# Kernel optimization log

Hardware: AMD Instinct MI355X
Metric: run time of the kernel (lower is better)

The kernel has to match this reference:

```python
import jax, jax.numpy as jnp
import numpy as np

N_NODES = 65536
N_FEAT = 64
N_EDGES = 1048576
N_GRAPHS = 16
LP_ITERS = 30


def setup_inputs() -> dict:
    key = jax.random.key(0)
    k1, k2, k3 = jax.random.split(key, 3)
    x = jax.random.normal(k1, (N_NODES, N_FEAT), dtype=jnp.float32)
    edge_index = jax.random.randint(k2, (2, N_EDGES), 0, N_NODES, dtype=jnp.int32)
    batch = jnp.sort(jax.random.randint(k3, (N_NODES,), 0, N_GRAPHS, dtype=jnp.int32))
    v2 = jnp.full((1,), 3.5, dtype=jnp.float32)  # learnable affinity scale param
    return {"x": x, "edge_index": edge_index, "batch": batch, "v2": v2}


def _lp_clustering(row, col, aff, n_nodes, n_iters):
    """Label propagation: each node adopts the neighbor label with max summed affinity."""
    E = row.shape[0]
    aff = jax.lax.stop_gradient(aff)  # clustering is discrete, no grad path

    def body(_, labels):
        lab_c = labels[col]                                    # neighbor labels per edge
        order = jnp.lexsort((lab_c, row))                      # sort by (row, neighbor-label)
        r_s, l_s, w_s = row[order], lab_c[order], aff[order]
        new_grp = jnp.concatenate([jnp.ones((1,), bool),
                                   (r_s[1:] != r_s[:-1]) | (l_s[1:] != l_s[:-1])])
        gid = jnp.cumsum(new_grp) - 1                          # dense (row,label) group ids
        gsum = jax.ops.segment_sum(w_s, gid, num_segments=E)   # affinity mass per group
        gcnt = jax.ops.segment_sum(jnp.ones_like(w_s), gid, num_segments=E)
        valid = gcnt > 0
        g_row = jnp.where(valid, jax.ops.segment_max(r_s, gid, num_segments=E), 0)
        g_lab = jnp.where(valid, jax.ops.segment_max(l_s, gid, num_segments=E), n_nodes)
        node_max = jax.ops.segment_max(jnp.where(valid, gsum, -jnp.inf), g_row,
                                       num_segments=n_nodes)
        win = valid & (gsum == node_max[g_row])
        # smallest winning label == torch argmax first-hit tie-break
        return jax.ops.segment_min(jnp.where(win, g_lab, n_nodes), g_row,
                                   num_segments=n_nodes)

    labels0 = jnp.arange(n_nodes, dtype=row.dtype)
    return jax.lax.fori_loop(0, n_iters, body, labels0)


def _forward(x, edge_index, batch, v2):
    n = x.shape[0]
    loops = jnp.arange(n, dtype=edge_index.dtype)
    ei = jnp.concatenate([edge_index, jnp.stack([loops, loops])], axis=1)  # add_self_loops
    row, col = ei[0], ei[1]

    # P2-style affinities: log_aff = -v2 * ||x_i - x_j||^2 ; forward exponentiates
    sqdist = jnp.sum((x[row] - x[col]) ** 2, axis=1)  # [E]
    losses = jnp.mean(sqdist)
    aff = jnp.exp(-v2[0] * sqdist)

    node_labels = _lp_clustering(row, col, aff, n, LP_ITERS)

    # unique(return_inverse): dense relabel of surviving cluster ids (sorted order)
    present = jnp.zeros((n,), jnp.int32).at[node_labels].set(1)
    cluster_labels = (jnp.cumsum(present) - 1)[node_labels]

    # max_pool_x: scatter-max node features into clusters (padded to n rows)
    cx = jax.ops.segment_max(x, cluster_labels, num_segments=n)
    cb = jax.ops.segment_max(batch, cluster_labels, num_segments=n)
    nonempty = jax.ops.segment_sum(jnp.ones((n,), jnp.int32), cluster_labels,
                                   num_segments=n) > 0
    cx = jnp.where(nonempty[:, None], cx, 0.0)
    cb = jnp.where(nonempty, cb, -1)

    # coalesce(cluster_labels[edge_index]): sort + dedupe, duplicates padded with -1
    mr, mc = cluster_labels[row], cluster_labels[col]
    order = jnp.lexsort((mc, mr))
    mr_s, mc_s = mr[order], mc[order]
    dup = jnp.concatenate([jnp.zeros((1,), bool),
                           (mr_s[1:] == mr_s[:-1]) & (mc_s[1:] == mc_s[:-1])])
    cei = jnp.stack([jnp.where(dup, -1, mr_s), jnp.where(dup, -1, mc_s)])

    return cx, cei, cb, cluster_labels, losses


def reference(x, edge_index, batch, v2):
    return _forward(x, edge_index, batch, v2)
```

## Files before the change

### kernel.cpp

```cpp
#include <hip/hip_runtime.h>
#include <hip/hip_cooperative_groups.h>

namespace cg = cooperative_groups;

#define DI __device__ __forceinline__

constexpr int NN   = 65536;
constexpr int NF   = 64;
constexpr int E0c  = 1048576;
constexpr int ET   = E0c + NN;
constexpr int LPITERS = 30;
constexpr int KPOS = 16;
constexpr int MSCH = 4096;
constexpr int NCHK = ET / MSCH;
constexpr int SCAP = 8192;
constexpr int CAP0 = 6144;
constexpr int BPB  = CAP0 / 64;
constexpr int NPART2 = 256 * BPB;

constexpr int O_CX   = 0;
constexpr int O_CEI0 = NN * NF;
constexpr int O_CEI1 = O_CEI0 + ET;
constexpr int O_CB   = O_CEI0 + 2 * ET;
constexpr int O_CL   = O_CB + NN;
constexpr int O_LOSS = O_CL + NN;

constexpr int W_CHG   = 0;
constexpr int W_NCLUS = 32;
constexpr int W_H1    = 64;
constexpr int W_GC0   = W_H1 + 256;
constexpr int W_GC1   = W_GC0 + 256;
constexpr int W_SCP   = 832;
constexpr int W_SCO   = W_SCP + 256;
constexpr int W_PART  = W_SCO + 256;
constexpr int W_PCNT  = W_PART + NPART2;
constexpr int W_PCOL  = W_PCNT + NN;
constexpr int W_PW    = W_PCOL + NN*KPOS;
constexpr int W_L0    = W_PW + NN*KPOS;
constexpr int W_L1    = W_L0 + NN;
constexpr int W_PRES  = W_L1 + NN;
constexpr int W_PSUM  = W_PRES + NN;
constexpr int W_CLU   = W_PSUM + NN;
constexpr int W_CBA   = W_CLU + NN;
constexpr int W_K0    = W_CBA + NN;
constexpr int W_K1    = W_K0 + 256*CAP0;

DI void edge_rc(const int* ei, int e, int& r, int& c) {
  if (e < E0c) { r = ei[e]; c = ei[E0c + e]; }
  else         { r = e - E0c; c = r; }
}

DI unsigned fenc(float f) {
  unsigned u = __float_as_uint(f);
  return (u & 0x80000000u) ? ~u : (u | 0x80000000u);
}
DI float fdec(unsigned u) {
  u = (u & 0x80000000u) ? (u & 0x7fffffffu) : ~u;
  return __uint_as_float(u);
}

DI int lp_step(int r, int d, int c0, int c1, float q0, float q1,
               const int* __restrict__ pcol, const float* __restrict__ pw,
               const int* __restrict__ lin) {
  int bl = NN;
  if (d == 1) {
    bl = lin[c0];
  } else if (d == 2) {
    int l0 = lin[c0], l1 = lin[c1];
    if (l0 == l1) bl = l0;
    else if (q1 > q0 || (q1 == q0 && l1 < l0)) bl = l1;
    else bl = l0;
  } else if (d > 2) {
    float best = 0.f;
    for (int i = 0; i < d; ++i) {
      int li = lin[pcol[r * KPOS + i]];
      bool dup = false;
      for (int j = 0; j < i; ++j)
        if (lin[pcol[r * KPOS + j]] == li) { dup = true; break; }
      if (dup) continue;
      float sum = 0.f;
      for (int j = i; j < d; ++j)
        if (lin[pcol[r * KPOS + j]] == li) sum += pw[r * KPOS + j];
      if (sum > best || (sum == best && li < bl)) { best = sum; bl = li; }
    }
  }
  return bl;
}


__global__ __launch_bounds__(256) void init_small(int* ws) {
  for (int i = threadIdx.x; i < 832; i += 256) ws[i] = 0;
}

__global__ __launch_bounds__(256) void emultisplit(const int* __restrict__ ei,
                                                   int* __restrict__ gcur0,
                                                   unsigned* __restrict__ K0,
                                                   int* __restrict__ pcnt,
                                                   int* __restrict__ L0) {
  __shared__ unsigned skey[MSCH];
  __shared__ unsigned short binid[MSCH];
  __shared__ int hl[256], ss[256], hs[256], hc[256], gb[256];
  int t = threadIdx.x;
  if (blockIdx.x < 256) {
    int rr = blockIdx.x * 256 + t;
    pcnt[rr] = 0;
    L0[rr] = rr;
  }
  hl[t] = 0; __syncthreads();
  int base = blockIdx.x * MSCH;
  unsigned mykey[MSCH / 256];
  #pragma unroll
  for (int k = 0; k < MSCH / 256; ++k) {
    int e = base + k * 256 + t;
    int r, c; edge_rc(ei, e, r, c);
    unsigned key = ((unsigned)r << 16) | (unsigned)c;
    mykey[k] = key;
    atomicAdd(&hl[key >> 24], 1);
  }
  __syncthreads();
  int v = hl[t];
  ss[t] = v; __syncthreads();
  for (int off = 1; off < 256; off <<= 1) {
    int u = (t >= off) ? ss[t - off] : 0;
    __syncthreads();
    ss[t] += u;
    __syncthreads();
  }
  int excl = ss[t] - v;
  hs[t] = excl;
  hc[t] = excl;
  gb[t] = t * CAP0 + ((v > 0) ? atomicAdd(&gcur0[t], v) : 0);
  for (int j = excl; j < excl + v; ++j) binid[j] = (unsigned short)t;
  __syncthreads();
  #pragma unroll
  for (int k = 0; k < MSCH / 256; ++k) {
    int b = mykey[k] >> 24;
    int slot = atomicAdd(&hc[b], 1);
    skey[slot] = mykey[k];
  }
  __syncthreads();
  for (int i = t; i < MSCH; i += 256) {
    int b = binid[i];
    int pos = gb[b] + (i - hs[b]);
    if (pos < (b + 1) * CAP0) K0[pos] = skey[i];
  }
}

__global__ __launch_bounds__(256) void edge_pos2(const float* __restrict__ x,
                                                 const unsigned* __restrict__ K0,
                                                 const int* __restrict__ gcur0,
                                                 const float* __restrict__ v2,
                                                 float* __restrict__ part,
                                                 int* __restrict__ pcnt,
                                                 int* __restrict__ pcol,
                                                 float* __restrict__ pw) {
  __shared__ float ls[16];
  int t = threadIdx.x, sub = t >> 4, lane = t & 15;
  int bkt = blockIdx.x / BPB;
  int off = (blockIdx.x % BPB) * 64;
  int cnt = gcur0[bkt];
  float w = v2[0];
  unsigned kk[4]; bool act[4];
  float4 A[4], B[4];
  #pragma unroll
  for (int q = 0; q < 4; ++q) {
    int j = off + sub * 4 + q;
    act[q] = (j < cnt);
    kk[q] = K0[bkt * CAP0 + (act[q] ? j : 0)];
  }
  #pragma unroll
  for (int q = 0; q < 4; ++q) {
    int r = kk[q] >> 16, c = kk[q] & 0xFFFF;
    A[q] = ((const float4*)(x + (size_t)r * NF))[lane];
    B[q] = ((const float4*)(x + (size_t)c * NF))[lane];
  }
  __builtin_amdgcn_sched_barrier(0);
  float lsum = 0.f;
  #pragma unroll
  for (int q = 0; q < 4; ++q) {
    float dx = A[q].x - B[q].x, dy = A[q].y - B[q].y;
    float dz = A[q].z - B[q].z, dw = A[q].w - B[q].w;
    float s = dx * dx + dy * dy + dz * dz + dw * dw;
    #pragma unroll
    for (int m = 1; m < 16; m <<= 1) s += __shfl_xor(s, m, 16);
    if (lane == 0 && act[q]) {
      lsum += s;
      float aff = expf(-w * s);
      if (aff > 0.f) {
        int r = kk[q] >> 16, c = kk[q] & 0xFFFF;
        int slot = atomicAdd(&pcnt[r], 1);
        if (slot < KPOS) { pcol[r * KPOS + slot] = c; pw[r * KPOS + slot] = aff; }
      }
    }
  }
  if (lane == 0) ls[sub] = lsum;
  __syncthreads();
  if (t == 0) {
    float s = 0.f;
    #pragma unroll
    for (int k = 0; k < 16; ++k) s += ls[k];
    part[blockIdx.x] = s;
  }
}

__global__ __launch_bounds__(256) void lp_iter0(const int* __restrict__ pcnt,
                                                const int* __restrict__ pcol,
                                                const float* __restrict__ pw,
                                                const int* __restrict__ L0,
                                                int* __restrict__ L1,
                                                int* __restrict__ chg,
                                                const float* __restrict__ part,
                                                float* __restrict__ out_loss) {
  __shared__ float smf[256];
  int t = threadIdx.x;
  int r = blockIdx.x * 256 + t;
  int d = pcnt[r];
  if (d > KPOS) d = KPOS;
  int c0 = 0, c1 = 0; float q0 = 0.f, q1 = 0.f;
  if (d >= 1) { c0 = pcol[r * KPOS];     q0 = pw[r * KPOS]; }
  if (d >= 2) { c1 = pcol[r * KPOS + 1]; q1 = pw[r * KPOS + 1]; }
  int bl = lp_step(r, d, c0, c1, q0, q1, pcol, pw, L0);
  L1[r] = bl;
  if (bl != L0[r]) atomicOr(&chg[0], 1);
  if (blockIdx.x == 0) {
    float s = 0.f;
    for (int i = t; i < NPART2; i += 256) s += part[i];
    smf[t] = s; __syncthreads();
    for (int off = 128; off; off >>= 1) {
      if (t < off) smf[t] += smf[t + off];
      __syncthreads();
    }
    if (t == 0) out_loss[0] = smf[0] / (float)ET;
  }
}

__global__ __launch_bounds__(256) void general_tail(
    const int* __restrict__ pcnt, const int* __restrict__ pcol,
    const float* __restrict__ pw, int* __restrict__ L0, int* __restrict__ L1,
    int* __restrict__ chg, int* __restrict__ pres, int* __restrict__ psum,
    int* __restrict__ clu, float* __restrict__ out_cl, int* __restrict__ cba,
    unsigned* __restrict__ cxacc, const float* __restrict__ x,
    const int* __restrict__ batch, int* __restrict__ nclus_g,
    int* __restrict__ scp, int* __restrict__ sco, int* __restrict__ h1,
    const int* __restrict__ gcur0, int* __restrict__ gcur1,
    const unsigned* __restrict__ K0, unsigned* __restrict__ K1,
    float* __restrict__ out_cb) {
  if (chg[0] == 0) return;
  __shared__ int sm[256], hl[256], bases[256];
  __shared__ int sbc;
  cg::grid_group grid = cg::this_grid();
  int t = threadIdx.x, b = blockIdx.x;
  int r = b * 256 + t;
  pres[r] = 0;
  cba[r] = -1;
  {
    uint4 z = make_uint4(0u, 0u, 0u, 0u);
    uint4* p = (uint4*)(cxacc + ((size_t)r << 6));
    #pragma unroll
    for (int q = 0; q < 16; ++q) p[q] = z;
  }
  int mylab = L1[r];
  int d = pcnt[r]; if (d > KPOS) d = KPOS;
  int c0 = 0, c1 = 0; float q0 = 0.f, q1 = 0.f;
  if (d >= 1) { c0 = pcol[r * KPOS];     q0 = pw[r * KPOS]; }
  if (d >= 2) { c1 = pcol[r * KPOS + 1]; q1 = pw[r * KPOS + 1]; }
  for (int it = 1; it < LPITERS; ++it) {
    const int* lin = (it & 1) ? L1 : L0;
    int* lout = (it & 1) ? L0 : L1;
    int bl = lp_step(r, d, c0, c1, q0, q1, pcol, pw, lin);
    lout[r] = bl;
    if (bl != mylab) atomicOr(&chg[it], 1);
    mylab = bl;
    grid.sync();
    if (t == 0) sbc = *(volatile int*)&chg[it];
    __syncthreads();
    if (sbc == 0) break;
  }
  L0[r] = mylab;
  grid.sync();
  pres[mylab] = 1;
  grid.sync();
  int v = pres[r];
  sm[t] = v; __syncthreads();
  for (int off = 1; off < 256; off <<= 1) {
    int u = (t >= off) ? sm[t - off] : 0;
    __syncthreads();
    sm[t] += u;
    __syncthreads();
  }
  int lexcl = sm[t] - v;
  if (t == 255) scp[b] = sm[255];
  grid.sync();
  if (b == 0) {
    int p = scp[t];
    sm[t] = p; __syncthreads();
    for (int off = 1; off < 256; off <<= 1) {
      int u = (t >= off) ? sm[t - off] : 0;
      __syncthreads();
      sm[t] += u;
      __syncthreads();
    }
    sco[t] = sm[t] - p;
    if (t == 255) nclus_g[0] = sm[255];
  }
  grid.sync();
  psum[r] = lexcl + sco[b];
  grid.sync();
  int cr = psum[mylab];
  clu[r] = cr;
  out_cl[r] = (float)cr;
  grid.sync();
  for (int f = 0; f < 64; ++f)
    atomicMax(&cxacc[((size_t)cr << 6) + f], fenc(x[((size_t)r << 6) + f]));
  atomicMax(&cba[cr], batch[r]);
  grid.sync();
  int ncl = nclus_g[0];
  for (int f = 0; f < 64; ++f) {
    unsigned u = cxacc[((size_t)r << 6) + f];
    ((float*)cxacc)[((size_t)r << 6) + f] = (r < ncl) ? fdec(u) : 0.f;
  }
  out_cb[r] = (float)cba[r];
  hl[t] = 0; __syncthreads();
  int cnt = gcur0[b];
  for (int i = t; i < cnt; i += 256) {
    unsigned k = K0[b * CAP0 + i];
    atomicAdd(&hl[((unsigned)clu[k >> 16]) >> 8], 1);
  }
  __syncthreads();
  if (hl[t]) atomicAdd(&h1[t], hl[t]);
  grid.sync();
  int hv = h1[t];
  sm[t] = hv; __syncthreads();
  for (int off = 1; off < 256; off <<= 1) {
    int u = (t >= off) ? sm[t - off] : 0;
    __syncthreads();
    sm[t] += u;
    __syncthreads();
  }
  bases[t] = sm[t] - hv;
  __syncthreads();
  for (int i = t; i < cnt; i += 256) {
    unsigned k = K0[b * CAP0 + i];
    unsigned k1 = ((unsigned)clu[k >> 16] << 16) | (unsigned)clu[k & 0xFFFF];
    int b1 = k1 >> 24;
    int pos = bases[b1] + atomicAdd(&gcur1[b1], 1);
    K1[pos] = k1;
  }
}

__global__ __launch_bounds__(512) void sortwrite(unsigned* __restrict__ K0,
                                                 const int* __restrict__ gcur0,
                                                 unsigned* __restrict__ K1,
                                                 const int* __restrict__ h1,
                                                 const int* __restrict__ chg,
                                                 const float4* __restrict__ x4,
                                                 const int* __restrict__ batch,
                                                 float4* __restrict__ out_cx4,
                                                 float* __restrict__ out_cl,
                                                 float* __restrict__ out_cb,
                                                 float* __restrict__ o0,
                                                 float* __restrict__ o1) {
  __shared__ unsigned sk[SCAP];
  __shared__ int hl[256], ss[256], sbs[257], cur[256], sh[2];
  int t = threadIdx.x, b = blockIdx.x;
  bool fast = (chg[0] == 0);
  if (fast) {
    int base4 = b * (256 * 16);
    for (int i = t; i < 256 * 16; i += 512) out_cx4[base4 + i] = x4[base4 + i];
    int rbase = b * 256;
    for (int i = t; i < 256; i += 512) {
      out_cl[rbase + i] = (float)(rbase + i);
      out_cb[rbase + i] = (float)batch[rbase + i];
    }
  }
  const int* cnts = fast ? gcur0 : h1;
  if (t < 256) ss[t] = cnts[t];
  __syncthreads();
  for (int off = 1; off < 256; off <<= 1) {
    int u = (t < 256 && t >= off) ? ss[t - off] : 0;
    __syncthreads();
    if (t < 256) ss[t] += u;
    __syncthreads();
  }
  if (t == 0) { sh[0] = ss[b] - cnts[b]; sh[1] = cnts[b]; }
  __syncthreads();
  int sout = sh[0], d = sh[1];
  if (d <= 0) return;
  unsigned* kp = fast ? (K0 + b * CAP0) : (K1 + sout);
  if (d <= SCAP) {
    if (t < 256) hl[t] = 0;
    __syncthreads();
    for (int i = t; i < d; i += 512)
      atomicAdd(&hl[(kp[i] >> 16) & 0xFF], 1);
    __syncthreads();
    if (t < 256) ss[t] = hl[t];
    __syncthreads();
    for (int off = 1; off < 256; off <<= 1) {
      int u = (t < 256 && t >= off) ? ss[t - off] : 0;
      __syncthreads();
      if (t < 256) ss[t] += u;
      __syncthreads();
    }
    if (t < 256) { sbs[t] = ss[t] - hl[t]; cur[t] = ss[t] - hl[t]; }
    if (t == 255) sbs[256] = d;
    __syncthreads();
    for (int i = t; i < d; i += 512) {
      unsigned k = kp[i];
      int slot = atomicAdd(&cur[(k >> 16) & 0xFF], 1);
      sk[slot] = k;
    }
    __syncthreads();
    int wave = t >> 6, lane = t & 63;
    for (int sb = wave; sb < 256; sb += 8) {
      int s0 = sbs[sb], s1 = sbs[sb + 1], dd = s1 - s0;
      if (dd <= 1) continue;
      if (dd <= 64) {
        unsigned k = (lane < dd) ? sk[s0 + lane] : 0xFFFFFFFFu;
        #pragma unroll
        for (int size = 2; size <= 64; size <<= 1) {
          #pragma unroll
          for (int stride = size >> 1; stride > 0; stride >>= 1) {
            unsigned o = __shfl_xor(k, stride, 64);
            bool takeMin = (((lane & stride) == 0) == ((lane & size) == 0));
            unsigned mn = k < o ? k : o, mx = k < o ? o : k;
            k = takeMin ? mn : mx;
          }
        }
        if (lane < dd) sk[s0 + lane] = k;
      } else if (lane == 0) {
        for (int i = s0 + 1; i < s1; ++i) {
          unsigned k = sk[i];
          int j = i - 1;
          while (j >= s0 && sk[j] > k) { sk[j + 1] = sk[j]; --j; }
          sk[j + 1] = k;
        }
      }
    }
    __syncthreads();
    for (int i = t; i < d; i += 512) {
      unsigned k = sk[i];
      bool dup = (i > 0) && (sk[i - 1] == k);
      o0[sout + i] = dup ? -1.f : (float)(k >> 16);
      o1[sout + i] = dup ? -1.f : (float)(k & 0xffffu);
    }
  } else {
    if (t == 0) {
      for (int i = 1; i < d; ++i) {
        unsigned k = kp[i];
        int j = i - 1;
        while (j >= 0 && kp[j] > k) { kp[j + 1] = kp[j]; --j; }
        kp[j + 1] = k;
      }
    }
    __syncthreads();
    for (int i = t; i < d; i += 512) {
      unsigned k = kp[i];
      bool dup = (i > 0) && (kp[i - 1] == k);
      o0[sout + i] = dup ? -1.f : (float)(k >> 16);
      o1[sout + i] = dup ? -1.f : (float)(k & 0xffffu);
    }
  }
}


extern "C" void kernel_launch(void* const* d_in, const int* in_sizes, int n_in,
                              void* d_out, int out_size, void* d_ws, size_t ws_size,
                              hipStream_t stream) {
  const float* x   = (const float*)d_in[0];
  const int* ei    = (const int*)d_in[1];
  const int* batch = (const int*)d_in[2];
  const float* v2  = (const float*)d_in[3];
  float* out = (float*)d_out;
  int* ws = (int*)d_ws;
  unsigned* cxacc = (unsigned*)(out + O_CX);

  init_small<<<1, 256, 0, stream>>>(ws);

  emultisplit<<<NCHK, 256, 0, stream>>>(ei, ws + W_GC0, (unsigned*)(ws + W_K0),
                                        ws + W_PCNT, ws + W_L0);

  edge_pos2<<<NPART2, 256, 0, stream>>>(x, (const unsigned*)(ws + W_K0),
                                        ws + W_GC0, v2, (float*)(ws + W_PART),
                                        ws + W_PCNT, ws + W_PCOL, (float*)(ws + W_PW));

  lp_iter0<<<NN / 256, 256, 0, stream>>>(ws + W_PCNT, ws + W_PCOL,
                                         (const float*)(ws + W_PW),
                                         ws + W_L0, ws + W_L1, ws + W_CHG,
                                         (const float*)(ws + W_PART), out + O_LOSS);

  {
    const int* pcnt = ws + W_PCNT;
    const int* pcol = ws + W_PCOL;
    const float* pw = (const float*)(ws + W_PW);
    int* L0 = ws + W_L0;
    int* L1 = ws + W_L1;
    int* chg = ws + W_CHG;
    int* pres = ws + W_PRES;
    int* psum = ws + W_PSUM;
    int* clu = ws + W_CLU;
    float* out_cl = out + O_CL;
    int* cba = ws + W_CBA;
    unsigned* cxa = cxacc;
    const float* x_ = x;
    const int* batch_ = batch;
    int* nclus_g = ws + W_NCLUS;
    int* scp = ws + W_SCP;
    int* sco = ws + W_SCO;
    int* h1 = ws + W_H1;
    const int* gcur0 = ws + W_GC0;
    int* gcur1 = ws + W_GC1;
    const unsigned* K0 = (const unsigned*)(ws + W_K0);
    unsigned* K1 = (unsigned*)(ws + W_K1);
    float* out_cb = out + O_CB;
    void* args[] = { (void*)&pcnt, (void*)&pcol, (void*)&pw,
                     (void*)&L0, (void*)&L1, (void*)&chg, (void*)&pres,
                     (void*)&psum, (void*)&clu, (void*)&out_cl, (void*)&cba,
                     (void*)&cxa, (void*)&x_, (void*)&batch_, (void*)&nclus_g,
                     (void*)&scp, (void*)&sco, (void*)&h1, (void*)&gcur0,
                     (void*)&gcur1, (void*)&K0, (void*)&K1, (void*)&out_cb };
    hipLaunchCooperativeKernel((const void*)general_tail, dim3(NN / 256),
                               dim3(256), args, 0, stream);
  }

  sortwrite<<<256, 512, 0, stream>>>((unsigned*)(ws + W_K0), ws + W_GC0,
                                     (unsigned*)(ws + W_K1), ws + W_H1,
                                     ws + W_CHG, (const float4*)x, batch,
                                     (float4*)(out + O_CX), out + O_CL,
                                     out + O_CB, out + O_CEI0, out + O_CEI1);
}
```

Before: 170.6 us.

## Gather fp16 copy of node features for edge distance computation

Converts x to packed half2 inside the multisplit kernel, storing it in the output's cx region as scratch. The edge-distance kernel then gathers 16-byte fp16 rows with 8 lanes per edge instead of fp32 rows with 16 lanes, halving gather traffic. It also exits empty blocks early and forces self-loop distances to zero. The cost is reduced precision in the squared distances, computed with fp16 arithmetic, which can shift affinities and break ties in label propagation. It also relies on cx being overwritten later.

```diff
diff --git a/kernel.cpp b/kernel.cpp
--- a/kernel.cpp
+++ b/kernel.cpp
@@ -1,4 +1,5 @@
 #include <hip/hip_runtime.h>
+#include <hip/hip_fp16.h>
 #include <hip/hip_cooperative_groups.h>
 
 namespace cg = cooperative_groups;
@@ -96,7 +97,9 @@
                                                    int* __restrict__ gcur0,
                                                    unsigned* __restrict__ K0,
                                                    int* __restrict__ pcnt,
-                                                   int* __restrict__ L0) {
+                                                   int* __restrict__ L0,
+                                                   const float2* __restrict__ x2,
+                                                   unsigned* __restrict__ xh) {
   __shared__ unsigned skey[MSCH];
   __shared__ unsigned short binid[MSCH];
   __shared__ int hl[256], ss[256], hs[256], hc[256], gb[256];
@@ -105,6 +108,11 @@
     int rr = blockIdx.x * 256 + t;
     pcnt[rr] = 0;
     L0[rr] = rr;
+  }
+  for (int i = blockIdx.x * 256 + t; i < NN * NF / 2; i += NCHK * 256) {
+    float2 f = x2[i];
+    __half2 h = __floats2half2_rn(f.x, f.y);
+    xh[i] = *reinterpret_cast<unsigned*>(&h);
   }
   hl[t] = 0; __syncthreads();
   int base = blockIdx.x * MSCH;
@@ -146,7 +154,7 @@
   }
 }
 
-__global__ __launch_bounds__(256) void edge_pos2(const float* __restrict__ x,
+__global__ __launch_bounds__(256) void edge_pos2(const unsigned* __restrict__ xh,
                                                  const unsigned* __restrict__ K0,
                                                  const int* __restrict__ gcur0,
                                                  const float* __restrict__ v2,
@@ -154,51 +162,62 @@
                                                  int* __restrict__ pcnt,
                                                  int* __restrict__ pcol,
                                                  float* __restrict__ pw) {
-  __shared__ float ls[16];
-  int t = threadIdx.x, sub = t >> 4, lane = t & 15;
+  __shared__ float ls[32];
+  int t = threadIdx.x, grp = t >> 3, lane = t & 7;
   int bkt = blockIdx.x / BPB;
   int off = (blockIdx.x % BPB) * 64;
   int cnt = gcur0[bkt];
+  if (off >= cnt) {
+    if (t == 0) part[blockIdx.x] = 0.f;
+    return;
+  }
   float w = v2[0];
-  unsigned kk[4]; bool act[4];
-  float4 A[4], B[4];
+  unsigned kk[2]; bool act[2];
+  uint4 A[2], B[2];
   #pragma unroll
-  for (int q = 0; q < 4; ++q) {
-    int j = off + sub * 4 + q;
+  for (int q = 0; q < 2; ++q) {
+    int j = off + grp * 2 + q;
     act[q] = (j < cnt);
     kk[q] = K0[bkt * CAP0 + (act[q] ? j : 0)];
   }
   #pragma unroll
-  for (int q = 0; q < 4; ++q) {
+  for (int q = 0; q < 2; ++q) {
     int r = kk[q] >> 16, c = kk[q] & 0xFFFF;
-    A[q] = ((const float4*)(x + (size_t)r * NF))[lane];
-    B[q] = ((const float4*)(x + (size_t)c * NF))[lane];
+    A[q] = ((const uint4*)(xh + (size_t)r * 32))[lane];
+    B[q] = ((const uint4*)(xh + (size_t)c * 32))[lane];
   }
   __builtin_amdgcn_sched_barrier(0);
   float lsum = 0.f;
   #pragma unroll
-  for (int q = 0; q < 4; ++q) {
-    float dx = A[q].x - B[q].x, dy = A[q].y - B[q].y;
-    float dz = A[q].z - B[q].z, dw = A[q].w - B[q].w;
-    float s = dx * dx + dy * dy + dz * dz + dw * dw;
-    #pragma unroll
-    for (int m = 1; m < 16; m <<= 1) s += __shfl_xor(s, m, 16);
+  for (int q = 0; q < 2; ++q) {
+    const __half2* ah = reinterpret_cast<const __half2*>(&A[q]);
+    const __half2* bh = reinterpret_cast<const __half2*>(&B[q]);
+    __half2 d0 = __hsub2(ah[0], bh[0]);
+    __half2 acc = __hmul2(d0, d0);
+    __half2 d1 = __hsub2(ah[1], bh[1]); acc = __hfma2(d1, d1, acc);
+    __half2 d2 = __hsub2(ah[2], bh[2]); acc = __hfma2(d2, d2, acc);
+    __half2 d3 = __hsub2(ah[3], bh[3]); acc = __hfma2(d3, d3, acc);
+    float s = __low2float(acc) + __high2float(acc);
+    s += __shfl_xor(s, 1, 8);
+    s += __shfl_xor(s, 2, 8);
+    s += __shfl_xor(s, 4, 8);
     if (lane == 0 && act[q]) {
+      int r = kk[q] >> 16, c = kk[q] & 0xFFFF;
+      if (r == c) s = 0.f;
       lsum += s;
       float aff = expf(-w * s);
       if (aff > 0.f) {
-        int r = kk[q] >> 16, c = kk[q] & 0xFFFF;
         int slot = atomicAdd(&pcnt[r], 1);
         if (slot < KPOS) { pcol[r * KPOS + slot] = c; pw[r * KPOS + slot] = aff; }
       }
     }
   }
-  if (lane == 0) ls[sub] = lsum;
+  if (lane == 0) ls[grp] = lsum;
   __syncthreads();
   if (t == 0) {
     float s = 0.f;
     #pragma unroll
-    for (int k = 0; k < 16; ++k) s += ls[k];
+    for (int k = 0; k < 32; ++k) s += ls[k];
     part[blockIdx.x] = s;
   }
 }
@@ -473,13 +492,15 @@
   float* out = (float*)d_out;
   int* ws = (int*)d_ws;
   unsigned* cxacc = (unsigned*)(out + O_CX);
+  unsigned* xh = cxacc;
 
   init_small<<<1, 256, 0, stream>>>(ws);
 
   emultisplit<<<NCHK, 256, 0, stream>>>(ei, ws + W_GC0, (unsigned*)(ws + W_K0),
-                                        ws + W_PCNT, ws + W_L0);
-
-  edge_pos2<<<NPART2, 256, 0, stream>>>(x, (const unsigned*)(ws + W_K0),
+                                        ws + W_PCNT, ws + W_L0,
+                                        (const float2*)x, xh);
+
+  edge_pos2<<<NPART2, 256, 0, stream>>>(xh, (const unsigned*)(ws + W_K0),
                                         ws + W_GC0, v2, (float*)(ws + W_PART),
                                         ws + W_PCNT, ws + W_PCOL, (float*)(ws + W_PW));
 
```

Result: faster. 157.6 us (-7.6%).
